# Kernel optimization log

Hardware: AMD Instinct MI355X
Metric: run time of the kernel (lower is better)

## Reference

```python
import jax, jax.numpy as jnp
import numpy as np

DIM = 768
HEADS = 12
DIM_HEAD = DIM // HEADS
SEQ = 1024
BATCH = 16
DEPTH = 6
MAX_DEPTH = 12
ALPHA = 0.5


def _decomposed_kernel(n, depth, alpha, max_depth, inverse):
    # symmetric (inverse) matrix square root of the OU-process kernel matrix
    if depth == 0:
        return np.eye(n, dtype=np.float32)
    gamma = -0.5 * np.log(1.0 - alpha ** (2.0 * depth / max_depth))
    ar = np.arange(n, dtype=np.float64)
    K = np.exp(-gamma * np.abs(ar[:, None] - ar[None, :]))
    w, V = np.linalg.eigh(K)
    thr = w.max() * n * np.finfo(w.dtype).eps
    s = np.clip(w, thr, None)
    s = 1.0 / np.sqrt(s) if inverse else np.sqrt(s)
    return ((V * s[None, :]) @ V.T).astype(np.float32)


def _make_buffers():
    prev_inv = _decomposed_kernel(SEQ, DEPTH - 1, ALPHA, MAX_DEPTH, inverse=True)
    cur = _decomposed_kernel(SEQ, DEPTH, ALPHA, MAX_DEPTH, inverse=False)
    A = (cur @ prev_inv).astype(np.float32)
    mn = A.min()
    if mn <= 0:
        A = np.clip(A, abs(mn) + np.finfo(np.float32).eps, None)
    row_sum = A.sum(1)                      # (N,)
    B = np.log(A / row_sum)                 # broadcast over last axis (matches torch)
    d = row_sum.reshape(1, 1, SEQ, 1).astype(np.float32)
    return jnp.asarray(d), jnp.asarray(B[None, None]).astype(jnp.float32)


def setup_inputs() -> dict:
    key = jax.random.key(0)
    kx, kw = jax.random.split(key)
    x = jax.random.normal(kx, (BATCH, SEQ, DIM), dtype=jnp.float32)
    # module zeros the q block; use normal(std=dim^-0.5) everywhere for a non-degenerate test
    w_qkv = jax.random.normal(kw, (3 * DIM, DIM), dtype=jnp.float32) * (DIM ** -0.5)
    b_qkv = jnp.zeros((3 * DIM,), dtype=jnp.float32)
    d, b_bias = _make_buffers()
    return {"x": x, "w_qkv": w_qkv, "b_qkv": b_qkv, "d": d, "b_bias": b_bias}


def reference(x, w_qkv, b_qkv, d, b_bias):
    B, N, D = x.shape
    qkv = x @ w_qkv.T + b_qkv                                   # (B,N,3D)
    qkv = qkv.reshape(B, N, 3, HEADS, DIM_HEAD).transpose(2, 0, 3, 1, 4)
    q, k, v = qkv[0], qkv[1], qkv[2]                            # (B,H,N,dh)
    scale = DIM_HEAD ** -0.5
    scores = jnp.einsum("bhnd,bhmd->bhnm", q, k) * scale + b_bias
    attn = jax.nn.softmax(scores, axis=-1)
    out = d * jnp.einsum("bhnm,bhmd->bhnd", attn, v)            # post-softmax row scale
    return out.transpose(0, 2, 1, 3).reshape(B, N, D)
```

## Files before the change

kernel.cpp:

```cpp
#include <hip/hip_runtime.h>
#include <cstdint>
#include <cstddef>

typedef __attribute__((ext_vector_type(8))) short short8;
typedef __attribute__((ext_vector_type(4))) short short4_;
typedef __attribute__((ext_vector_type(4))) float f32x4;
typedef __attribute__((ext_vector_type(2))) unsigned int uint2_;

__device__ inline unsigned short bf16rne(float f) {
    uint32_t u = __builtin_bit_cast(uint32_t, f);
    u += 0x7fffu + ((u >> 16) & 1u);
    return (unsigned short)(u >> 16);
}

#define GLDS(g, l)                                                              \
    __builtin_amdgcn_global_load_lds(                                           \
        (const __attribute__((address_space(1))) void*)(g),                     \
        (__attribute__((address_space(3))) void*)(l), 16, 0, 0)

__global__ void cvt_kernel(const float* __restrict__ src,
                           unsigned short* __restrict__ dst, int n8) {
    int i = blockIdx.x * blockDim.x + threadIdx.x;
    if (i >= n8) return;
    const float4* s = (const float4*)src + (size_t)i * 2;
    float4 a = s[0], b = s[1];
    uint32_t w0 = bf16rne(a.x) | ((uint32_t)bf16rne(a.y) << 16);
    uint32_t w1 = bf16rne(a.z) | ((uint32_t)bf16rne(a.w) << 16);
    uint32_t w2 = bf16rne(b.x) | ((uint32_t)bf16rne(b.y) << 16);
    uint32_t w3 = bf16rne(b.z) | ((uint32_t)bf16rne(b.w) << 16);
    uint4 o; o.x = w0; o.y = w1; o.z = w2; o.w = w3;
    ((uint4*)dst)[i] = o;
}

__global__ __launch_bounds__(256) void qkv_gemm(
    const unsigned short* __restrict__ X, const unsigned short* __restrict__ W,
    const float* __restrict__ bqkv,
    unsigned short* __restrict__ qo, unsigned short* __restrict__ ko,
    unsigned short* __restrict__ vo)
{
    __shared__ unsigned short smem[16896];
    unsigned short* As = smem;
    unsigned short* Bs = smem + 8192;

    const int tid  = threadIdx.x;
    const int m0   = blockIdx.y * 128;
    const int n0   = blockIdx.x * 128;
    const int wid  = tid >> 6;
    const int lane = tid & 63;
    const int m16  = lane & 15;
    const int quad = lane >> 4;
    const int wm   = wid >> 1, wn = wid & 1;

    f32x4 acc[4][4];
    #pragma unroll
    for (int i = 0; i < 4; i++)
        #pragma unroll
        for (int j = 0; j < 4; j++) acc[i][j] = (f32x4){0.f, 0.f, 0.f, 0.f};

    for (int kt = 0; kt < 12; ++kt) {
        const int k0 = kt * 64;
        #pragma unroll
        for (int rd = 0; rd < 4; ++rd) {
            int id = rd * 256 + tid;
            int row = id >> 3, c = id & 7;
            GLDS(X + (size_t)(m0 + row) * 768 + k0 + c * 8, &As[id * 8]);
        }
        #pragma unroll
        for (int rd = 0; rd < 4; ++rd) {
            int id = rd * 256 + tid;
            int row = id >> 3, c = id & 7;
            GLDS(W + (size_t)(n0 + row) * 768 + k0 + c * 8, &Bs[id * 8]);
        }
        __syncthreads();
        #pragma unroll
        for (int ks = 0; ks < 2; ++ks) {
            short8 a[4], b[4];
            #pragma unroll
            for (int mb = 0; mb < 4; mb++)
                a[mb] = *(const short8*)&As[(wm * 64 + mb * 16 + m16) * 64 + ks * 32 + quad * 8];
            #pragma unroll
            for (int nb = 0; nb < 4; nb++)
                b[nb] = *(const short8*)&Bs[(wn * 64 + nb * 16 + m16) * 64 + ks * 32 + quad * 8];
            #pragma unroll
            for (int mb = 0; mb < 4; mb++)
                #pragma unroll
                for (int nb = 0; nb < 4; nb++)
                    acc[mb][nb] = __builtin_amdgcn_mfma_f32_16x16x32_bf16(
                        a[mb], b[nb], acc[mb][nb], 0, 0, 0);
        }
        __syncthreads();
    }

    float bias_n[4];
    #pragma unroll
    for (int nb = 0; nb < 4; nb++) bias_n[nb] = bqkv[n0 + wn * 64 + nb * 16 + m16];

    const int which = n0 / 768;
    const int hbase = (n0 % 768) / 64;
    const int bI  = m0 >> 10;
    const int ns0 = m0 & 1023;

    if (which == 2) {
        #pragma unroll
        for (int mb = 0; mb < 4; ++mb)
            #pragma unroll
            for (int nb = 0; nb < 4; ++nb) {
                int n  = wn * 64 + nb * 16 + m16;
                int hh = hbase + (n >> 6);
                int d  = n & 63;
                int pos = ns0 + wm * 64 + mb * 16 + quad * 4;
                short4_ v4;
                #pragma unroll
                for (int r = 0; r < 4; ++r)
                    v4[r] = (short)bf16rne(acc[mb][nb][r] + bias_n[nb]);
                *(short4_*)(vo + ((size_t)(bI * 12 + hh) * 64 + d) * 1024 + pos) = v4;
            }
        return;
    }

    #pragma unroll
    for (int mb = 0; mb < 4; mb++)
        #pragma unroll
        for (int nb = 0; nb < 4; nb++)
            #pragma unroll
            for (int r = 0; r < 4; r++) {
                float v = acc[mb][nb][r] + bias_n[nb];
                smem[(wm * 64 + mb * 16 + quad * 4 + r) * 132 + wn * 64 + nb * 16 + m16] =
                    bf16rne(v);
            }
    __syncthreads();

    unsigned short* outp = (which == 0) ? qo : ko;
    #pragma unroll
    for (int rd = 0; rd < 8; ++rd) {
        int id = rd * 256 + tid;
        int row = id >> 4, c = id & 15;
        short4_ lo = *(const short4_*)&smem[row * 132 + c * 8];
        short4_ hi = *(const short4_*)&smem[row * 132 + c * 8 + 4];
        short8 v8 = __builtin_shufflevector(lo, hi, 0, 1, 2, 3, 4, 5, 6, 7);
        int h  = hbase + (c >> 3);
        int dc = (c & 7) * 8;
        unsigned short* dst =
            outp + ((size_t)(bI * 12 + h) * 1024 + ns0 + row) * 64 + dc;
        *(short8*)dst = v8;
    }
}

__global__ __launch_bounds__(256, 5) void attn_kernel(
    const unsigned short* __restrict__ Q, const unsigned short* __restrict__ K,
    const unsigned short* __restrict__ Vt, const float* __restrict__ bias,
    const float* __restrict__ dvec, float* __restrict__ out, int nbh8)
{
    __shared__ unsigned short Ks[8192];
    __shared__ unsigned short Vs[8192];

    const int tid  = threadIdx.x;
    const int wid  = tid >> 6;
    const int lane = tid & 63;
    const int m16  = lane & 15;
    const int quad = lane >> 4;

    const int f    = blockIdx.x;
    const int xcd  = f & 7;
    const int r_   = f >> 3;
    const int qt   = r_ & 15;
    const int bhl  = r_ >> 4;
    const int bh   = xcd * nbh8 + bhl;
    const int b = bh / 12, h = bh % 12;
    const int q0 = qt * 64;
    const int qrow = q0 + wid * 16 + m16;

    const unsigned short* Qb = Q  + (size_t)bh * 65536;
    const unsigned short* Kb = K  + (size_t)bh * 65536;
    const unsigned short* Vb = Vt + (size_t)bh * 65536;

    int k_src[4], v_src[4];
    #pragma unroll
    for (int rd = 0; rd < 4; ++rd) {
        int id = rd * 256 + tid;
        int pos = id >> 3, dbs = id & 7;
        int db = dbs ^ (pos & 7);
        k_src[rd] = pos * 64 + db * 8;
        int pb = id >> 6, d = id & 63;
        v_src[rd] = d * 1024 + pb * 8;
    }

    short8 qf0 = *(const short8*)(Qb + (size_t)qrow * 64 + quad * 8);
    short8 qf1 = *(const short8*)(Qb + (size_t)qrow * 64 + 32 + quad * 8);

    f32x4 acc[4];
    #pragma unroll
    for (int nb = 0; nb < 4; nb++) acc[nb] = (f32x4){0.f, 0.f, 0.f, 0.f};
    float m_i = -3.0e38f, l_i = 0.f;

    for (int kv = 0; kv < 8; ++kv) {
        const int k0 = kv * 128;
        #pragma unroll
        for (int rd = 0; rd < 4; ++rd)
            GLDS(Kb + (size_t)k0 * 64 + k_src[rd], &Ks[(rd * 256 + tid) * 8]);
        #pragma unroll
        for (int rd = 0; rd < 4; ++rd)
            GLDS(Vb + (size_t)k0 + v_src[rd], &Vs[(rd * 256 + tid) * 8]);
        __syncthreads();

        f32x4 sc[8];
        #pragma unroll
        for (int cb = 0; cb < 8; ++cb) sc[cb] = (f32x4){0.f, 0.f, 0.f, 0.f};
        #pragma unroll
        for (int ks = 0; ks < 2; ++ks) {
            #pragma unroll
            for (int cb = 0; cb < 8; ++cb) {
                int pos = cb * 16 + m16;
                int slot = pos * 8 + ((ks * 4 + quad) ^ (m16 & 7));
                short8 a = *(const short8*)&Ks[slot * 8];
                sc[cb] = __builtin_amdgcn_mfma_f32_16x16x32_bf16(
                    a, (ks == 0) ? qf0 : qf1, sc[cb], 0, 0, 0);
            }
        }

        float mx = -3.0e38f;
        #pragma unroll
        for (int cb = 0; cb < 8; ++cb) {
            float4 bv = *(const float4*)(bias + (size_t)qrow * 1024 + k0 + cb * 16 + quad * 4);
            sc[cb][0] = sc[cb][0] * 0.125f + bv.x;
            sc[cb][1] = sc[cb][1] * 0.125f + bv.y;
            sc[cb][2] = sc[cb][2] * 0.125f + bv.z;
            sc[cb][3] = sc[cb][3] * 0.125f + bv.w;
            mx = fmaxf(mx, fmaxf(fmaxf(sc[cb][0], sc[cb][1]), fmaxf(sc[cb][2], sc[cb][3])));
        }
        mx = fmaxf(mx, __shfl_xor(mx, 16, 64));
        mx = fmaxf(mx, __shfl_xor(mx, 32, 64));
        float mnew = fmaxf(m_i, mx);
        float al = __expf(m_i - mnew);
        m_i = mnew;

        float rs = 0.f;
        short4_ pf[8];
        #pragma unroll
        for (int cb = 0; cb < 8; ++cb) {
            float p0 = __expf(sc[cb][0] - m_i);
            float p1 = __expf(sc[cb][1] - m_i);
            float p2 = __expf(sc[cb][2] - m_i);
            float p3 = __expf(sc[cb][3] - m_i);
            rs += (p0 + p1) + (p2 + p3);
            uint2_ pd;
            pd[0] = __builtin_amdgcn_perm(__builtin_bit_cast(uint32_t, p1),
                                          __builtin_bit_cast(uint32_t, p0), 0x07060302u);
            pd[1] = __builtin_amdgcn_perm(__builtin_bit_cast(uint32_t, p3),
                                          __builtin_bit_cast(uint32_t, p2), 0x07060302u);
            pf[cb] = __builtin_bit_cast(short4_, pd);
        }
        rs += __shfl_xor(rs, 16, 64);
        rs += __shfl_xor(rs, 32, 64);
        l_i = l_i * al + rs;
        #pragma unroll
        for (int nb = 0; nb < 4; nb++) {
            acc[nb][0] *= al; acc[nb][1] *= al;
            acc[nb][2] *= al; acc[nb][3] *= al;
        }

        #pragma unroll
        for (int ks = 0; ks < 8; ++ks) {
            #pragma unroll
            for (int nb = 0; nb < 4; ++nb) {
                int slot = (ks * 2 + (quad >> 1)) * 64 + nb * 16 + m16;
                short4_ av = *(const short4_*)&Vs[slot * 8 + (quad & 1) * 4];
                acc[nb] = __builtin_amdgcn_mfma_f32_16x16x16bf16_1k(av, pf[ks], acc[nb], 0, 0, 0);
            }
        }
        __syncthreads();
    }

    float scl = dvec[qrow] / l_i;
    #pragma unroll
    for (int nb = 0; nb < 4; ++nb) {
        float4 o;
        o.x = acc[nb][0] * scl; o.y = acc[nb][1] * scl;
        o.z = acc[nb][2] * scl; o.w = acc[nb][3] * scl;
        *(float4*)(out + ((size_t)b * 1024 + qrow) * 768 + h * 64 + nb * 16 + quad * 4) = o;
    }
}

extern "C" void kernel_launch(void* const* d_in, const int* in_sizes, int n_in,
                              void* d_out, int out_size, void* d_ws, size_t ws_size,
                              hipStream_t stream) {
    const float* x     = (const float*)d_in[0];
    const float* w     = (const float*)d_in[1];
    const float* bqkv  = (const float*)d_in[2];
    const float* dvec  = (const float*)d_in[3];
    const float* bbias = (const float*)d_in[4];
    float* out = (float*)d_out;

    char* ws = (char*)d_ws;
    unsigned short* wb = (unsigned short*)ws;
    unsigned short* xb = (unsigned short*)((char*)d_out + 25165824);

    cvt_kernel<<<6144, 256, 0, stream>>>(x, xb, 1572864);
    cvt_kernel<<<864, 256, 0, stream>>>(w, wb, 221184);

    const size_t NEED_FULL = 3538944ull + 3ull * 25165824ull;
    if (ws_size >= NEED_FULL) {
        unsigned short* qb = (unsigned short*)(ws + 3538944);
        unsigned short* kb = qb + 12582912;
        unsigned short* vb = kb + 12582912;
        qkv_gemm<<<dim3(18, 128), 256, 0, stream>>>(xb, wb, bqkv, qb, kb, vb);
        attn_kernel<<<3072, 256, 0, stream>>>(qb, kb, vb, bbias, dvec, out, 24);
    } else {
        unsigned short* qb = (unsigned short*)(ws + 3538944);
        unsigned short* kb = qb + 3145728;
        unsigned short* vb = kb + 3145728;
        for (int c = 0; c < 4; ++c) {
            const unsigned short* xc = xb + (size_t)c * 3145728;
            qkv_gemm<<<dim3(18, 32), 256, 0, stream>>>(xc, wb, bqkv, qb, kb, vb);
            attn_kernel<<<768, 256, 0, stream>>>(
                qb, kb, vb, bbias, dvec, out + (size_t)c * 3145728, 6);
        }
    }
}
```

Baseline: 377.1 us.

## Double-buffer K/V tiles with 64-key blocks and prefetch bias; skip no-op rescale

The attention loop now uses two 64-key LDS buffers instead of one 128-key buffer. The next K/V tile and the next bias values are issued before the current tile is computed, so global loads overlap with MFMA and softmax work. The online-softmax rescale of acc and l_i is skipped when no lane's running max increases. The cost is twice as many iterations, each followed by a barrier, and more live registers for the prefetched bias, which could hurt occupancy under launch_bounds(256,5).

```diff
diff --git a/kernel.cpp b/kernel.cpp
--- a/kernel.cpp
+++ b/kernel.cpp
@@ -151,8 +151,8 @@
     const unsigned short* __restrict__ Vt, const float* __restrict__ bias,
     const float* __restrict__ dvec, float* __restrict__ out, int nbh8)
 {
-    __shared__ unsigned short Ks[8192];
-    __shared__ unsigned short Vs[8192];
+    __shared__ unsigned short Ks[2][4096];
+    __shared__ unsigned short Vs[2][4096];
 
     const int tid  = threadIdx.x;
     const int wid  = tid >> 6;
@@ -173,10 +173,11 @@
     const unsigned short* Qb = Q  + (size_t)bh * 65536;
     const unsigned short* Kb = K  + (size_t)bh * 65536;
     const unsigned short* Vb = Vt + (size_t)bh * 65536;
-
-    int k_src[4], v_src[4];
-    #pragma unroll
-    for (int rd = 0; rd < 4; ++rd) {
+    const float* brow = bias + (size_t)qrow * 1024 + quad * 4;
+
+    int k_src[2], v_src[2];
+    #pragma unroll
+    for (int rd = 0; rd < 2; ++rd) {
         int id = rd * 256 + tid;
         int pos = id >> 3, dbs = id & 7;
         int db = dbs ^ (pos & 7);
@@ -193,26 +194,46 @@
     for (int nb = 0; nb < 4; nb++) acc[nb] = (f32x4){0.f, 0.f, 0.f, 0.f};
     float m_i = -3.0e38f, l_i = 0.f;
 
-    for (int kv = 0; kv < 8; ++kv) {
-        const int k0 = kv * 128;
-        #pragma unroll
-        for (int rd = 0; rd < 4; ++rd)
-            GLDS(Kb + (size_t)k0 * 64 + k_src[rd], &Ks[(rd * 256 + tid) * 8]);
-        #pragma unroll
-        for (int rd = 0; rd < 4; ++rd)
-            GLDS(Vb + (size_t)k0 + v_src[rd], &Vs[(rd * 256 + tid) * 8]);
-        __syncthreads();
-
-        f32x4 sc[8];
-        #pragma unroll
-        for (int cb = 0; cb < 8; ++cb) sc[cb] = (f32x4){0.f, 0.f, 0.f, 0.f};
+    #pragma unroll
+    for (int rd = 0; rd < 2; ++rd)
+        GLDS(Kb + k_src[rd], &Ks[0][(rd * 256 + tid) * 8]);
+    #pragma unroll
+    for (int rd = 0; rd < 2; ++rd)
+        GLDS(Vb + v_src[rd], &Vs[0][(rd * 256 + tid) * 8]);
+    float4 bv[4];
+    #pragma unroll
+    for (int cb = 0; cb < 4; ++cb) bv[cb] = *(const float4*)(brow + cb * 16);
+    __syncthreads();
+
+    for (int kv = 0; kv < 16; ++kv) {
+        const int cur = kv & 1;
+        const int k0n = (kv + 1) * 64;
+
+        float4 bvn[4];
+        if (kv < 15) {
+            #pragma unroll
+            for (int rd = 0; rd < 2; ++rd)
+                GLDS(Kb + (size_t)k0n * 64 + k_src[rd],
+                     &Ks[cur ^ 1][(rd * 256 + tid) * 8]);
+            #pragma unroll
+            for (int rd = 0; rd < 2; ++rd)
+                GLDS(Vb + (size_t)k0n + v_src[rd],
+                     &Vs[cur ^ 1][(rd * 256 + tid) * 8]);
+            #pragma unroll
+            for (int cb = 0; cb < 4; ++cb)
+                bvn[cb] = *(const float4*)(brow + k0n + cb * 16);
+        }
+
+        f32x4 sc[4];
+        #pragma unroll
+        for (int cb = 0; cb < 4; ++cb) sc[cb] = (f32x4){0.f, 0.f, 0.f, 0.f};
         #pragma unroll
         for (int ks = 0; ks < 2; ++ks) {
             #pragma unroll
-            for (int cb = 0; cb < 8; ++cb) {
+            for (int cb = 0; cb < 4; ++cb) {
                 int pos = cb * 16 + m16;
                 int slot = pos * 8 + ((ks * 4 + quad) ^ (m16 & 7));
-                short8 a = *(const short8*)&Ks[slot * 8];
+                short8 a = *(const short8*)&Ks[cur][slot * 8];
                 sc[cb] = __builtin_amdgcn_mfma_f32_16x16x32_bf16(
                     a, (ks == 0) ? qf0 : qf1, sc[cb], 0, 0, 0);
             }
@@ -220,24 +241,32 @@
 
         float mx = -3.0e38f;
         #pragma unroll
-        for (int cb = 0; cb < 8; ++cb) {
-            float4 bv = *(const float4*)(bias + (size_t)qrow * 1024 + k0 + cb * 16 + quad * 4);
-            sc[cb][0] = sc[cb][0] * 0.125f + bv.x;
-            sc[cb][1] = sc[cb][1] * 0.125f + bv.y;
-            sc[cb][2] = sc[cb][2] * 0.125f + bv.z;
-            sc[cb][3] = sc[cb][3] * 0.125f + bv.w;
+        for (int cb = 0; cb < 4; ++cb) {
+            sc[cb][0] = sc[cb][0] * 0.125f + bv[cb].x;
+            sc[cb][1] = sc[cb][1] * 0.125f + bv[cb].y;
+            sc[cb][2] = sc[cb][2] * 0.125f + bv[cb].z;
+            sc[cb][3] = sc[cb][3] * 0.125f + bv[cb].w;
             mx = fmaxf(mx, fmaxf(fmaxf(sc[cb][0], sc[cb][1]), fmaxf(sc[cb][2], sc[cb][3])));
         }
         mx = fmaxf(mx, __shfl_xor(mx, 16, 64));
         mx = fmaxf(mx, __shfl_xor(mx, 32, 64));
-        float mnew = fmaxf(m_i, mx);
-        float al = __expf(m_i - mnew);
-        m_i = mnew;
+
+        if (!__all(mx <= m_i)) {
+            float mnew = fmaxf(m_i, mx);
+            float al = __expf(m_i - mnew);
+            m_i = mnew;
+            l_i *= al;
+            #pragma unroll
+            for (int nb = 0; nb < 4; nb++) {
+                acc[nb][0] *= al; acc[nb][1] *= al;
+                acc[nb][2] *= al; acc[nb][3] *= al;
+            }
+        }
 
         float rs = 0.f;
-        short4_ pf[8];
-        #pragma unroll
-        for (int cb = 0; cb < 8; ++cb) {
+        short4_ pf[4];
+        #pragma unroll
+        for (int cb = 0; cb < 4; ++cb) {
             float p0 = __expf(sc[cb][0] - m_i);
             float p1 = __expf(sc[cb][1] - m_i);
             float p2 = __expf(sc[cb][2] - m_i);
@@ -252,23 +281,23 @@
         }
         rs += __shfl_xor(rs, 16, 64);
         rs += __shfl_xor(rs, 32, 64);
-        l_i = l_i * al + rs;
-        #pragma unroll
-        for (int nb = 0; nb < 4; nb++) {
-            acc[nb][0] *= al; acc[nb][1] *= al;
-            acc[nb][2] *= al; acc[nb][3] *= al;
-        }
-
-        #pragma unroll
-        for (int ks = 0; ks < 8; ++ks) {
+        l_i += rs;
+
+        #pragma unroll
+        for (int ks = 0; ks < 4; ++ks) {
             #pragma unroll
             for (int nb = 0; nb < 4; ++nb) {
                 int slot = (ks * 2 + (quad >> 1)) * 64 + nb * 16 + m16;
-                short4_ av = *(const short4_*)&Vs[slot * 8 + (quad & 1) * 4];
+                short4_ av = *(const short4_*)&Vs[cur][slot * 8 + (quad & 1) * 4];
                 acc[nb] = __builtin_amdgcn_mfma_f32_16x16x16bf16_1k(av, pf[ks], acc[nb], 0, 0, 0);
             }
         }
+
         __syncthreads();
+        if (kv < 15) {
+            #pragma unroll
+            for (int cb = 0; cb < 4; ++cb) bv[cb] = bvn[cb];
+        }
     }
 
     float scl = dvec[qrow] / l_i;
```

After: 360.1 us. 1.05x faster.
